# Kernel optimization log

Hardware: AMD Instinct MI355X
Metric: run time of the kernel (lower is better)

The kernel has to match this reference:

```python
import jax, jax.numpy as jnp
import numpy as np

B, S, D, H, F = 2, 2048, 1024, 16, 4096
DH = D // H  # per-head dim = 64
EPS = 1e-5


def _layer_norm(x, g, b):
    mu = jnp.mean(x, axis=-1, keepdims=True)
    var = jnp.mean((x - mu) ** 2, axis=-1, keepdims=True)
    return (x - mu) * jax.lax.rsqrt(var + EPS) * g + b


def _mha(q_in, kv_in, wq, bq, wk, bk, wv, bv, wo, bo, causal):
    b, s, d = q_in.shape
    q = (q_in @ wq + bq).reshape(b, s, H, DH).transpose(0, 2, 1, 3)
    k = (kv_in @ wk + bk).reshape(b, s, H, DH).transpose(0, 2, 1, 3)
    v = (kv_in @ wv + bv).reshape(b, s, H, DH).transpose(0, 2, 1, 3)
    scores = jnp.einsum('bhqd,bhkd->bhqk', q, k) / np.sqrt(DH).astype(np.float32)
    if causal:
        mask = jnp.tril(jnp.ones((s, s), dtype=bool))
        scores = jnp.where(mask, scores, -jnp.inf)
    attn = jax.nn.softmax(scores, axis=-1)
    out = jnp.einsum('bhqk,bhkd->bhqd', attn, v)
    out = out.transpose(0, 2, 1, 3).reshape(b, s, d)
    return out @ wo + bo


def setup_inputs() -> dict:
    key = jax.random.key(0)
    ks = iter(jax.random.split(key, 24))
    def w(shape, fan_in):
        return jax.random.normal(next(ks), shape, jnp.float32) / np.sqrt(fan_in).astype(np.float32)
    inp = {
        'encoder_output': jax.random.normal(next(ks), (B, S, D), jnp.float32),
        'decoder_input': jax.random.normal(next(ks), (B, S, D), jnp.float32),
    }
    for pre in ('sa', 'ca'):
        for nm in ('wq', 'wk', 'wv', 'wo'):
            inp[f'{pre}_{nm}'] = w((D, D), D)
            inp[f'{pre}_b{nm[-1]}'] = jnp.zeros((D,), jnp.float32)
        inp[f'{pre}_g'] = jnp.ones((D,), jnp.float32)
        inp[f'{pre}_bt'] = jnp.zeros((D,), jnp.float32)
    inp['f_w1'] = w((D, F), D); inp['f_b1'] = jnp.zeros((F,), jnp.float32)
    inp['f_w2'] = w((F, D), F); inp['f_b2'] = jnp.zeros((D,), jnp.float32)
    inp['f_g'] = jnp.ones((D,), jnp.float32); inp['f_bt'] = jnp.zeros((D,), jnp.float32)
    return inp


def reference(encoder_output, decoder_input,
              sa_wq, sa_bq, sa_wk, sa_bk, sa_wv, sa_bv, sa_wo, sa_bo, sa_g, sa_bt,
              ca_wq, ca_bq, ca_wk, ca_bk, ca_wv, ca_bv, ca_wo, ca_bo, ca_g, ca_bt,
              f_w1, f_b1, f_w2, f_b2, f_g, f_bt):
    # masked self-attention + residual + LN
    x = _mha(decoder_input, decoder_input, sa_wq, sa_bq, sa_wk, sa_bk, sa_wv, sa_bv, sa_wo, sa_bo, True)
    x = _layer_norm(x + decoder_input, sa_g, sa_bt)
    # encoder-decoder attention + residual + LN
    y = _mha(x, encoder_output, ca_wq, ca_bq, ca_wk, ca_bk, ca_wv, ca_bv, ca_wo, ca_bo, False)
    y = _layer_norm(y + x, ca_g, ca_bt)
    # FFN + residual + LN
    h = jax.nn.relu(y @ f_w1 + f_b1) @ f_w2 + f_b2
    return _layer_norm(h + y, f_g, f_bt)
```

## Files before the change

kernel.cpp:

```cpp
#include <hip/hip_runtime.h>
#include <hip/hip_bf16.h>


typedef __attribute__((ext_vector_type(8))) short bf16x8;
typedef __attribute__((ext_vector_type(4))) float f32x4;
typedef __attribute__((ext_vector_type(16))) float f32x16;

#define LOG2E 1.44269504088896340736f

constexpr int Bb = 2, Ss = 2048, Dd = 1024, Hh = 16, DHd = 64, Ff = 4096;
constexpr int Mrows = Bb * Ss;
constexpr int BHS = Bb * Hh * Ss;

static __device__ __forceinline__ ushort f2b(float f) {
    union { float f; unsigned u; } x{f};
    unsigned r = x.u + 0x7fffu + ((x.u >> 16) & 1u);
    return (ushort)(r >> 16);
}

static __device__ __forceinline__ unsigned pk2(float a, float b) {
    __hip_bfloat162 h = __float22bfloat162_rn(make_float2(a, b));
    unsigned u;
    __builtin_memcpy(&u, &h, 4);
    return u;
}

static __device__ __forceinline__ unsigned pk2t(float a, float b) {
    union { float f; unsigned u; } ua{a}, ub{b};
    return __builtin_amdgcn_perm(ub.u, ua.u, 0x07060302);
}

static __device__ __forceinline__ void gl2lds16(const void* g, void* l) {
    __builtin_amdgcn_global_load_lds(
        (const __attribute__((address_space(1))) void*)g,
        (__attribute__((address_space(3))) void*)l, 16, 0, 0);
}

__global__ __launch_bounds__(256) void cvt_kernel(const float* __restrict__ in,
                                                  ushort* __restrict__ out) {
    int i = (blockIdx.x * 256 + threadIdx.x) * 4;
    float4 v = *(const float4*)(in + i);
    ushort4 u;
    u.x = f2b(v.x); u.y = f2b(v.y); u.z = f2b(v.z); u.w = f2b(v.w);
    *(ushort4*)(out + i) = u;
}

__global__ __launch_bounds__(256) void wtrans_kernel(const float* __restrict__ w,
                                                     ushort* __restrict__ wT,
                                                     int K, int N) {
    __shared__ float t[32][33];
    int tx = threadIdx.x & 31, ty = threadIdx.x >> 5;
    int kb = blockIdx.y * 32, nb = blockIdx.x * 32;
#pragma unroll
    for (int i = 0; i < 4; i++)
        t[ty + i * 8][tx] = w[(size_t)(kb + ty + i * 8) * N + nb + tx];
    __syncthreads();
#pragma unroll
    for (int i = 0; i < 4; i++)
        wT[(size_t)(nb + ty + i * 8) * K + kb + tx] = f2b(t[tx][ty + i * 8]);
}

__global__ __launch_bounds__(256) void pack_bias(const float* __restrict__ a,
                                                 const float* __restrict__ b,
                                                 const float* __restrict__ c,
                                                 float* __restrict__ out) {
    int i = blockIdx.x * 256 + threadIdx.x;
    const float* src = a; int j = i;
    if (i >= 2048)      { src = c; j = i - 2048; }
    else if (i >= 1024) { src = b; j = i - 1024; }
    out[i] = src[j];
}

__global__ __launch_bounds__(256) void gemm_kernel(const ushort* __restrict__ A,
                                                   const ushort* __restrict__ BT,
                                                   const float* __restrict__ bias,
                                                   void* __restrict__ out,
                                                   int M, int N, int K, int klen,
                                                   int mode, int relu, float qsc,
                                                   int vwhich) {
    __shared__ __align__(16) ushort As[128 * 64];
    __shared__ __align__(16) ushort Bs[128 * 64];
    const int tid = threadIdx.x;
    const int lane = tid & 63, wave = tid >> 6;
    const int lr = lane & 15, quad = lane >> 4;
    const int wm = wave & 1, wn = wave >> 1;
    const int nwg = gridDim.x * gridDim.y;
    const int orig = blockIdx.y * gridDim.x + blockIdx.x;
    const int wg = (orig & 7) * (nwg >> 3) + (orig >> 3);
    const int m0 = (wg / gridDim.x) * 128, n0 = (wg % gridDim.x) * 128;
    const int kz = blockIdx.z;
    const int kstart = kz * klen;

    f32x4 acc[4][4];
#pragma unroll
    for (int i = 0; i < 4; i++)
#pragma unroll
        for (int j = 0; j < 4; j++) acc[i][j] = (f32x4){0.f, 0.f, 0.f, 0.f};

    const int srow = tid >> 3;
    const int gchunk = ((tid & 7) ^ (srow & 7)) * 8;
    const ushort* aBase = A + (size_t)(m0 + srow) * K + gchunk;
    const ushort* bBase = BT + (size_t)(n0 + srow) * K + gchunk;
    const size_t rowStep = (size_t)32 * K;

    const int slotA = ((quad) ^ (lr & 7)) * 8;
    const int slotB = ((4 + quad) ^ (lr & 7)) * 8;

    for (int k0 = kstart; k0 < kstart + klen; k0 += 64) {
#pragma unroll
        for (int c = 0; c < 4; c++) {
            gl2lds16(aBase + c * rowStep + k0, &As[c * 2048 + tid * 8]);
            gl2lds16(bBase + c * rowStep + k0, &Bs[c * 2048 + tid * 8]);
        }
        __syncthreads();
#pragma unroll
        for (int kk = 0; kk < 2; kk++) {
            const int slot = kk ? slotB : slotA;
            bf16x8 af[4], bfr[4];
#pragma unroll
            for (int i = 0; i < 4; i++)
                af[i] = *(const bf16x8*)&As[(wm * 64 + i * 16 + lr) * 64 + slot];
#pragma unroll
            for (int j = 0; j < 4; j++)
                bfr[j] = *(const bf16x8*)&Bs[(wn * 64 + j * 16 + lr) * 64 + slot];
#pragma unroll
            for (int i = 0; i < 4; i++)
#pragma unroll
                for (int j = 0; j < 4; j++)
                    acc[i][j] = __builtin_amdgcn_mfma_f32_16x16x32_bf16(af[i], bfr[j], acc[i][j], 0, 0, 0);
        }
        __syncthreads();
    }

#pragma unroll
    for (int j = 0; j < 4; j++) {
        int col = n0 + wn * 64 + j * 16 + lr;
        float bv = (bias && kz == 0) ? bias[col] : 0.f;
#pragma unroll
        for (int i = 0; i < 4; i++) {
            int row0 = m0 + wm * 64 + i * 16 + quad * 4;
            float v[4];
#pragma unroll
            for (int r = 0; r < 4; r++) {
                v[r] = acc[i][j][r] + bv;
                if (relu) v[r] = fmaxf(v[r], 0.f);
            }
            if (mode == 0) {
                float* op = (float*)out + (size_t)kz * M * N;
#pragma unroll
                for (int r = 0; r < 4; r++)
                    op[(size_t)(row0 + r) * N + col] = v[r];
            } else if (mode == 1) {
#pragma unroll
                for (int r = 0; r < 4; r++)
                    ((ushort*)out)[(size_t)(row0 + r) * N + col] = f2b(v[r]);
            } else {
                int which = col >> 10, n1 = col & 1023;
                int h = n1 >> 6, dh = n1 & 63;
                int b = row0 >> 11, s0 = row0 & 2047;
                size_t wbase = (size_t)which * (Bb * Hh * Ss * DHd);
                if (which == vwhich) {
                    uint2 pk;
                    pk.x = pk2(v[0], v[1]); pk.y = pk2(v[2], v[3]);
                    *(uint2*)((ushort*)out + wbase +
                              ((size_t)(b * Hh + h) * DHd + dh) * Ss + s0) = pk;
                } else {
                    float sc = (which == 0) ? qsc : 1.f;
#pragma unroll
                    for (int r = 0; r < 4; r++)
                        ((ushort*)out)[wbase + (((size_t)(b * Hh + h) * Ss + s0 + r) * DHd) + dh] =
                            f2b(v[r] * sc);
                }
            }
        }
    }
}

#define MFMAP(I0)                                                              \
    __builtin_amdgcn_s_setprio(1);                                             \
    _Pragma("unroll")                                                          \
    for (int j = 0; j < 4; j++) {                                              \
        acc[I0][j] = __builtin_amdgcn_mfma_f32_16x16x32_bf16(af[0][0], bfr[j][0], acc[I0][j], 0, 0, 0);         \
        acc[I0][j] = __builtin_amdgcn_mfma_f32_16x16x32_bf16(af[0][1], bfr[j][1], acc[I0][j], 0, 0, 0);         \
        acc[I0 + 1][j] = __builtin_amdgcn_mfma_f32_16x16x32_bf16(af[1][0], bfr[j][0], acc[I0 + 1][j], 0, 0, 0); \
        acc[I0 + 1][j] = __builtin_amdgcn_mfma_f32_16x16x32_bf16(af[1][1], bfr[j][1], acc[I0 + 1][j], 0, 0, 0); \
    }                                                                          \
    __builtin_amdgcn_s_setprio(0);

#define PHASE_READ_A(IB)                                                       \
    af[0][0] = *(const bf16x8*)&Ac[aoff0 + (IB) * 1024];                       \
    af[0][1] = *(const bf16x8*)&Ac[aoff1 + (IB) * 1024];                       \
    af[1][0] = *(const bf16x8*)&Ac[aoff0 + ((IB) + 1) * 1024];                 \
    af[1][1] = *(const bf16x8*)&Ac[aoff1 + ((IB) + 1) * 1024];

#define GTILE(PF)                                                              \
  {                                                                            \
    const ushort* Ac = &As[(t & 1) * 16384];                                   \
    const ushort* Bc = &Bs[(t & 1) * 16384];                                   \
    const int nb = (t & 1) ^ 1;                                                \
    const int kn = kstart + (t + 1) * 64;                                      \
    bf16x8 bfr[4][2], af[2][2];                                                \
                                                        \
    _Pragma("unroll")                                                          \
    for (int j = 0; j < 4; j++) {                                              \
        bfr[j][0] = *(const bf16x8*)&Bc[boff0 + j * 1024];                     \
        bfr[j][1] = *(const bf16x8*)&Bc[boff1 + j * 1024];                     \
    }                                                                          \
    PHASE_READ_A(0)                                                            \
    if (PF) { stB(nb, kn, 0); stB(nb, kn, 1); }                                \
    __builtin_amdgcn_s_barrier();                                              \
    asm volatile("s_waitcnt lgkmcnt(0)" ::: "memory");                         \
    MFMAP(0)                                                                   \
    __builtin_amdgcn_s_barrier();                                              \
                                                        \
    PHASE_READ_A(2)                                                            \
    if (PF) { stB(nb, kn, 2); stB(nb, kn, 3); }                                \
    __builtin_amdgcn_s_barrier();                                              \
    asm volatile("s_waitcnt lgkmcnt(0)" ::: "memory");                         \
    MFMAP(2)                                                                   \
    if (PF) asm volatile("s_waitcnt vmcnt(4)" ::: "memory");                   \
    else    asm volatile("s_waitcnt vmcnt(0)" ::: "memory");                   \
    __builtin_amdgcn_s_barrier();                                              \
                                                        \
    PHASE_READ_A(4)                                                            \
    if (PF) { stA(nb, kn, 0); stA(nb, kn, 2); }                                \
    __builtin_amdgcn_s_barrier();                                              \
    asm volatile("s_waitcnt lgkmcnt(0)" ::: "memory");                         \
    MFMAP(4)                                                                   \
    __builtin_amdgcn_s_barrier();                                              \
                                                        \
    PHASE_READ_A(6)                                                            \
    if (PF) { stA(nb, kn, 1); stA(nb, kn, 3); }                                \
    __builtin_amdgcn_s_barrier();                                              \
    asm volatile("s_waitcnt lgkmcnt(0)" ::: "memory");                         \
    MFMAP(6)                                                                   \
    if (PF) asm volatile("s_waitcnt vmcnt(2)" ::: "memory");                   \
    __builtin_amdgcn_s_barrier();                                              \
  }

__global__ __launch_bounds__(512) void gemm256(const ushort* __restrict__ A,
                                               const ushort* __restrict__ BT,
                                               const float* __restrict__ bias,
                                               void* __restrict__ out,
                                               int M, int N, int K, int klen,
                                               int mode, int relu, float qsc,
                                               int vwhich) {
    __shared__ __align__(16) ushort As[2 * 16384];
    __shared__ __align__(16) ushort Bs[2 * 16384];
    const int tid = threadIdx.x;
    const int lane = tid & 63, wave = tid >> 6;
    const int lr = lane & 15, quad = lane >> 4;
    const int wm = wave & 1, wn = wave >> 1;
    const int nwg = gridDim.x * gridDim.y;
    const int orig = blockIdx.y * gridDim.x + blockIdx.x;
    const int wg = (orig & 7) * (nwg >> 3) + (orig >> 3);
    const int m0 = (wg / gridDim.x) * 256, n0 = (wg % gridDim.x) * 256;
    const int kz = blockIdx.z;
    const int kstart = kz * klen;

    f32x4 acc[8][4];
#pragma unroll
    for (int i = 0; i < 8; i++)
#pragma unroll
        for (int j = 0; j < 4; j++) acc[i][j] = (f32x4){0.f, 0.f, 0.f, 0.f};

    const int srow = tid >> 3;
    const int gchunk = ((tid & 7) ^ (srow & 7)) * 8;
    const ushort* aBase = A + (size_t)(m0 + srow) * K + gchunk;
    const ushort* bBase = BT + (size_t)(n0 + srow) * K + gchunk;
    const size_t rowStep = (size_t)64 * K;

    auto stA = [&](int b, int kn, int c) {
        gl2lds16(aBase + (size_t)c * rowStep + kn, &As[b * 16384 + c * 4096 + tid * 8]);
    };
    auto stB = [&](int b, int kn, int c) {
        gl2lds16(bBase + (size_t)c * rowStep + kn, &Bs[b * 16384 + c * 4096 + tid * 8]);
    };

    const int aoff0 = (wm * 128 + lr) * 64 + (((0 * 4 + quad)) ^ (lr & 7)) * 8;
    const int aoff1 = (wm * 128 + lr) * 64 + (((1 * 4 + quad)) ^ (lr & 7)) * 8;
    const int boff0 = (wn * 64 + lr) * 64 + (((0 * 4 + quad)) ^ (lr & 7)) * 8;
    const int boff1 = (wn * 64 + lr) * 64 + (((1 * 4 + quad)) ^ (lr & 7)) * 8;

    stB(0, kstart, 0); stB(0, kstart, 1); stB(0, kstart, 2); stB(0, kstart, 3);
    stA(0, kstart, 0); stA(0, kstart, 2); stA(0, kstart, 1); stA(0, kstart, 3);
    asm volatile("s_waitcnt vmcnt(2)" ::: "memory");
    __builtin_amdgcn_s_barrier();

    const int nkt = klen >> 6;
    for (int t = 0; t < nkt - 1; t++) GTILE(1)
    { const int t = nkt - 1; GTILE(0) }

#pragma unroll
    for (int j = 0; j < 4; j++) {
        int col = n0 + wn * 64 + j * 16 + lr;
        float bv = (bias && kz == 0) ? bias[col] : 0.f;
#pragma unroll
        for (int i = 0; i < 8; i++) {
            int row0 = m0 + wm * 128 + i * 16 + quad * 4;
            float v[4];
#pragma unroll
            for (int r = 0; r < 4; r++) {
                v[r] = acc[i][j][r] + bv;
                if (relu) v[r] = fmaxf(v[r], 0.f);
            }
            if (mode == 0) {
                float* op = (float*)out + (size_t)kz * M * N;
#pragma unroll
                for (int r = 0; r < 4; r++)
                    op[(size_t)(row0 + r) * N + col] = v[r];
            } else if (mode == 1) {
#pragma unroll
                for (int r = 0; r < 4; r++)
                    ((ushort*)out)[(size_t)(row0 + r) * N + col] = f2b(v[r]);
            } else {
                int which = col >> 10, n1 = col & 1023;
                int h = n1 >> 6, dh = n1 & 63;
                int b = row0 >> 11, s0 = row0 & 2047;
                size_t wbase = (size_t)which * (Bb * Hh * Ss * DHd);
                if (which == vwhich) {
                    uint2 pk;
                    pk.x = pk2(v[0], v[1]); pk.y = pk2(v[2], v[3]);
                    *(uint2*)((ushort*)out + wbase +
                              ((size_t)(b * Hh + h) * DHd + dh) * Ss + s0) = pk;
                } else {
                    float sc = (which == 0) ? qsc : 1.f;
#pragma unroll
                    for (int r = 0; r < 4; r++)
                        ((ushort*)out)[wbase + (((size_t)(b * Hh + h) * Ss + s0 + r) * DHd) + dh] =
                            f2b(v[r] * sc);
                }
            }
        }
    }
}

__global__ __launch_bounds__(256, 2) void attn_kernel(const ushort* __restrict__ Q,
                                                      const ushort* __restrict__ Kg,
                                                      const ushort* __restrict__ VT,
                                                      float* __restrict__ Op0,
                                                      float* __restrict__ Op1,
                                                      float* __restrict__ Ml,
                                                      int causal) {
    __shared__ __align__(16) ushort Ks[64 * 64];
    __shared__ __align__(16) ushort Vs[64 * 64];
    const int tid = threadIdx.x;
    const int lane = tid & 63, w = tid >> 6;
    const int lr31 = lane & 31, hi = lane >> 5, l7 = lane & 7;
    const int hi4 = hi * 4;
    const int L = blockIdx.z * 256 + blockIdx.y * 8 + blockIdx.x;
    const int bh = (L & 7) | (((L >> 6) & 3) << 3);
    const int bx = (L >> 3) & 7;
    const int p = L >> 8;
    const int qt = causal ? (p ? bx : (7 - bx)) : bx;
    const size_t hb = (size_t)bh * Ss * DHd;
    const int qbase = qt * 256 + w * 64;

    bf16x8 qf[2][4];
#pragma unroll
    for (int qg = 0; qg < 2; qg++)
#pragma unroll
        for (int ks = 0; ks < 4; ks++)
            qf[qg][ks] = *(const bf16x8*)(Q + hb +
                (size_t)(qbase + qg * 32 + lr31) * DHd + ks * 16 + hi * 8);

    f32x16 o[2][2];
#pragma unroll
    for (int i = 0; i < 2; i++)
#pragma unroll
        for (int j = 0; j < 2; j++)
#pragma unroll
            for (int r = 0; r < 16; r++) o[i][j][r] = 0.f;
    float l0 = 0.f, l1 = 0.f;

    const int srow8 = tid >> 3, sslot = tid & 7;
    const int sswz = (sslot ^ (srow8 & 7)) * 8;
    const ushort* kSrc = Kg + hb + (size_t)srow8 * DHd + sswz;
    const ushort* vSrc = VT + hb + (size_t)srow8 * Ss + sswz;

    uint4 kr0, kr1, vr0, vr1;
    auto ldKV = [&](int k0) {
        kr0 = *(const uint4*)(kSrc + (size_t)(k0 +  0) * DHd);
        kr1 = *(const uint4*)(kSrc + (size_t)(k0 + 32) * DHd);
        vr0 = *(const uint4*)(vSrc + k0);
        vr1 = *(const uint4*)(vSrc + (size_t)32 * Ss + k0);
    };
    auto wrKV = [&]() {
        *(uint4*)&Ks[tid * 8]        = kr0;
        *(uint4*)&Ks[2048 + tid * 8] = kr1;
        *(uint4*)&Vs[tid * 8]        = vr0;
        *(uint4*)&Vs[2048 + tid * 8] = vr1;
    };

    int so[4];
#pragma unroll
    for (int ks = 0; ks < 4; ks++) so[ks] = ((ks * 2 + hi) ^ l7) * 8;

    const int ktEnd = causal ? (qt + 1) * 4 : (Ss / 64);

    ldKV(p * 64);
    wrKV();
    __syncthreads();

    for (int kt = p; kt < ktEnd; kt += 2) {
        const int k0 = kt * 64;
        const int pf = (kt + 2 < ktEnd);
        if (pf) ldKV((kt + 2) * 64);
        if (!causal || k0 <= qbase + 63) {
            bf16x8 pb[2][4];
            float ps0 = 0.f, ps1 = 0.f;
            const int maskT = causal && (k0 == qbase);
#pragma unroll
            for (int kg = 0; kg < 2; kg++) {
                bf16x8 kf[4];
#pragma unroll
                for (int ks = 0; ks < 4; ks++)
                    kf[ks] = *(const bf16x8*)&Ks[(kg * 32 + lr31) * 64 + so[ks]];
                f32x16 st[2];
#pragma unroll
                for (int qg = 0; qg < 2; qg++) {
#pragma unroll
                    for (int r = 0; r < 16; r++) st[qg][r] = 0.f;
#pragma unroll
                    for (int ks = 0; ks < 4; ks++)
                        st[qg] = __builtin_amdgcn_mfma_f32_32x32x16_bf16(
                            kf[ks], qf[qg][ks], st[qg], 0, 0, 0);
                }
                if (maskT) {
#pragma unroll
                    for (int r = 0; r < 16; r++) {
                        int klr = kg * 32 + (r & 3) + 8 * (r >> 2) + hi4;
                        st[0][r] = (klr > lr31) ? -1e30f : st[0][r];
                        st[1][r] = (klr > lr31 + 32) ? -1e30f : st[1][r];
                    }
                }
#pragma unroll
                for (int qg = 0; qg < 2; qg++) {
                    float pv[16];
#pragma unroll
                    for (int r = 0; r < 16; r++) {
                        pv[r] = __builtin_amdgcn_exp2f(fminf(st[qg][r], 88.f));
                        if (qg == 0) ps0 += pv[r]; else ps1 += pv[r];
                    }
#pragma unroll
                    for (int tt = 0; tt < 2; tt++) {
                        const int rb = tt * 8;
                        unsigned X0 = pk2t(pv[rb + 0], pv[rb + 1]);
                        unsigned X1 = pk2t(pv[rb + 2], pv[rb + 3]);
                        unsigned Y0 = pk2t(pv[rb + 4], pv[rb + 5]);
                        unsigned Y1 = pk2t(pv[rb + 6], pv[rb + 7]);
                        asm("v_permlane32_swap_b32 %0, %1" : "+v"(X0), "+v"(Y0));
                        asm("v_permlane32_swap_b32 %0, %1" : "+v"(X1), "+v"(Y1));
                        union { unsigned u[4]; bf16x8 v; } pw;
                        pw.u[0] = X0; pw.u[1] = X1; pw.u[2] = Y0; pw.u[3] = Y1;
                        pb[qg][kg * 2 + tt] = pw.v;
                    }
                }
            }
            l0 += ps0 + __shfl_xor(ps0, 32);
            l1 += ps1 + __shfl_xor(ps1, 32);
#pragma unroll
            for (int ks = 0; ks < 4; ks++) {
                bf16x8 av0 = *(const bf16x8*)&Vs[lr31 * 64 + so[ks]];
                bf16x8 av1 = *(const bf16x8*)&Vs[(32 + lr31) * 64 + so[ks]];
                o[0][0] = __builtin_amdgcn_mfma_f32_32x32x16_bf16(av0, pb[0][ks], o[0][0], 0, 0, 0);
                o[0][1] = __builtin_amdgcn_mfma_f32_32x32x16_bf16(av1, pb[0][ks], o[0][1], 0, 0, 0);
                o[1][0] = __builtin_amdgcn_mfma_f32_32x32x16_bf16(av0, pb[1][ks], o[1][0], 0, 0, 0);
                o[1][1] = __builtin_amdgcn_mfma_f32_32x32x16_bf16(av1, pb[1][ks], o[1][1], 0, 0, 0);
            }
        }
        if (pf) {
            __syncthreads();
            wrKV();
            __syncthreads();
        }
    }

    Ml[(size_t)p * BHS + (size_t)bh * Ss + qbase + lane] = (lane & 32) ? l1 : l0;
    float* Op = p ? Op1 : Op0;
#pragma unroll
    for (int qg = 0; qg < 2; qg++) {
        size_t ob = ((size_t)bh * Ss + qbase + qg * 32 + lr31) * 64;
#pragma unroll
        for (int dhg = 0; dhg < 2; dhg++)
#pragma unroll
            for (int rq = 0; rq < 4; rq++) {
                f32x4 t;
#pragma unroll
                for (int c = 0; c < 4; c++) t[c] = o[qg][dhg][rq * 4 + c];
                *(f32x4*)(Op + ob + dhg * 32 + rq * 8 + hi4) = t;
            }
    }
}

__global__ __launch_bounds__(256) void attn_combine(const float* __restrict__ Op0,
                                                    const float* __restrict__ Op1,
                                                    const float* __restrict__ Ml,
                                                    ushort* __restrict__ O) {
    int g = blockIdx.x * 256 + threadIdx.x;
    int q = g >> 4, seg = g & 15;
    float inv = 1.f / (Ml[q] + Ml[BHS + q]);
    f32x4 x = *(const f32x4*)(Op0 + (size_t)q * 64 + seg * 4);
    f32x4 y = *(const f32x4*)(Op1 + (size_t)q * 64 + seg * 4);
    int bh = q >> 11, sq = q & 2047, bb = bh >> 4, h = bh & 15;
    uint2 u;
    u.x = pk2((x[0] + y[0]) * inv, (x[1] + y[1]) * inv);
    u.y = pk2((x[2] + y[2]) * inv, (x[3] + y[3]) * inv);
    *(uint2*)(O + ((size_t)(bb * Ss + sq)) * Dd + h * 64 + seg * 4) = u;
}

__global__ __launch_bounds__(256) void ln_kernel(const float* __restrict__ a0,
                                                 const float* __restrict__ a1,
                                                 const float* __restrict__ a2,
                                                 const float* __restrict__ a3,
                                                 const float* __restrict__ resid,
                                                 const float* __restrict__ g,
                                                 const float* __restrict__ bt,
                                                 float* __restrict__ out32,
                                                 ushort* __restrict__ outb) {
    const int row = blockIdx.x, tid = threadIdx.x;
    const size_t base = (size_t)row * Dd + tid * 4;
    float4 av = *(const float4*)(a0 + base);
    if (a1) { float4 t = *(const float4*)(a1 + base); av.x += t.x; av.y += t.y; av.z += t.z; av.w += t.w; }
    if (a2) { float4 t = *(const float4*)(a2 + base); av.x += t.x; av.y += t.y; av.z += t.z; av.w += t.w; }
    if (a3) { float4 t = *(const float4*)(a3 + base); av.x += t.x; av.y += t.y; av.z += t.z; av.w += t.w; }
    float4 rv = *(const float4*)(resid + base);
    float x0 = av.x + rv.x, x1 = av.y + rv.y, x2 = av.z + rv.z, x3 = av.w + rv.w;
    float s = x0 + x1 + x2 + x3;
    float q = x0 * x0 + x1 * x1 + x2 * x2 + x3 * x3;
#pragma unroll
    for (int off = 1; off <= 32; off <<= 1) {
        s += __shfl_xor(s, off);
        q += __shfl_xor(q, off);
    }
    __shared__ float red[8];
    int wave = tid >> 6, lane = tid & 63;
    if (lane == 0) { red[wave] = s; red[4 + wave] = q; }
    __syncthreads();
    s = red[0] + red[1] + red[2] + red[3];
    q = red[4] + red[5] + red[6] + red[7];
    float mu = s * (1.f / Dd);
    float var = q * (1.f / Dd) - mu * mu;
    float rs = rsqrtf(var + 1e-5f);
    int col = tid * 4;
    float4 gv = *(const float4*)(g + col);
    float4 bv = *(const float4*)(bt + col);
    float y0 = (x0 - mu) * rs * gv.x + bv.x;
    float y1 = (x1 - mu) * rs * gv.y + bv.y;
    float y2 = (x2 - mu) * rs * gv.z + bv.z;
    float y3 = (x3 - mu) * rs * gv.w + bv.w;
    if (out32) *(float4*)(out32 + base) = make_float4(y0, y1, y2, y3);
    if (outb) {
        ushort4 u; u.x = f2b(y0); u.y = f2b(y1); u.z = f2b(y2); u.w = f2b(y3);
        *(ushort4*)(outb + base) = u;
    }
}

constexpr size_t OFF_XB     = 0;
constexpr size_t OFF_ENCB   = OFF_XB     + 8388608;
constexpr size_t OFF_QKVWT  = OFF_ENCB   + 8388608;
constexpr size_t OFF_CAWQT  = OFF_QKVWT  + 6291456;
constexpr size_t OFF_CAKVT  = OFF_CAWQT  + 2097152;
constexpr size_t OFF_SAWOT  = OFF_CAKVT  + 4194304;
constexpr size_t OFF_CAWOT  = OFF_SAWOT  + 2097152;
constexpr size_t OFF_FW1T   = OFF_CAWOT  + 2097152;
constexpr size_t OFF_FW2T   = OFF_FW1T   + 8388608;
constexpr size_t OFF_SABQKV = OFF_FW2T   + 8388608;
constexpr size_t OFF_CABKV  = OFF_SABQKV + 12288;
constexpr size_t OFF_QB     = OFF_CABKV  + 8192;
constexpr size_t OFF_KB     = OFF_QB     + 8388608;
constexpr size_t OFF_VB     = OFF_KB     + 8388608;
constexpr size_t OFF_ATTNO  = OFF_VB     + 8388608;
constexpr size_t OFF_F1     = OFF_ATTNO  + 8388608;
constexpr size_t OFF_F2     = OFF_F1     + 16777216;
constexpr size_t OFF_X1B    = OFF_F2     + 16777216;
constexpr size_t OFF_F3     = OFF_X1B    + 8388608;
constexpr size_t OFF_YB     = OFF_F3     + 16777216;
constexpr size_t OFF_H1B    = OFF_YB     + 8388608;

extern "C" void kernel_launch(void* const* d_in, const int* in_sizes, int n_in,
                              void* d_out, int out_size, void* d_ws, size_t ws_size,
                              hipStream_t stream) {
    const float* enc   = (const float*)d_in[0];
    const float* dec   = (const float*)d_in[1];
    const float* sa_wq = (const float*)d_in[2];
    const float* sa_bq = (const float*)d_in[3];
    const float* sa_wk = (const float*)d_in[4];
    const float* sa_bk = (const float*)d_in[5];
    const float* sa_wv = (const float*)d_in[6];
    const float* sa_bv = (const float*)d_in[7];
    const float* sa_wo = (const float*)d_in[8];
    const float* sa_bo = (const float*)d_in[9];
    const float* sa_g  = (const float*)d_in[10];
    const float* sa_bt = (const float*)d_in[11];
    const float* ca_wq = (const float*)d_in[12];
    const float* ca_bq = (const float*)d_in[13];
    const float* ca_wk = (const float*)d_in[14];
    const float* ca_bk = (const float*)d_in[15];
    const float* ca_wv = (const float*)d_in[16];
    const float* ca_bv = (const float*)d_in[17];
    const float* ca_wo = (const float*)d_in[18];
    const float* ca_bo = (const float*)d_in[19];
    const float* ca_g  = (const float*)d_in[20];
    const float* ca_bt = (const float*)d_in[21];
    const float* f_w1  = (const float*)d_in[22];
    const float* f_b1  = (const float*)d_in[23];
    const float* f_w2  = (const float*)d_in[24];
    const float* f_b2  = (const float*)d_in[25];
    const float* f_g   = (const float*)d_in[26];
    const float* f_bt  = (const float*)d_in[27];

    char* ws = (char*)d_ws;
    ushort* xb     = (ushort*)(ws + OFF_XB);
    ushort* encb   = (ushort*)(ws + OFF_ENCB);
    ushort* qkvwT  = (ushort*)(ws + OFF_QKVWT);
    ushort* cawqT  = (ushort*)(ws + OFF_CAWQT);
    ushort* cakvT  = (ushort*)(ws + OFF_CAKVT);
    ushort* sawoT  = (ushort*)(ws + OFF_SAWOT);
    ushort* cawoT  = (ushort*)(ws + OFF_CAWOT);
    ushort* fw1T   = (ushort*)(ws + OFF_FW1T);
    ushort* fw2T   = (ushort*)(ws + OFF_FW2T);
    float*  sabqkv = (float*)(ws + OFF_SABQKV);
    float*  cabkv  = (float*)(ws + OFF_CABKV);
    ushort* qb     = (ushort*)(ws + OFF_QB);
    ushort* kb     = (ushort*)(ws + OFF_KB);
    ushort* vbt    = (ushort*)(ws + OFF_VB);
    ushort* attno  = (ushort*)(ws + OFF_ATTNO);
    float*  f1     = (float*)(ws + OFF_F1);
    float*  f2     = (float*)(ws + OFF_F2);
    ushort* x1b    = (ushort*)(ws + OFF_X1B);
    float*  x1f    = (float*)(ws + OFF_F3);
    ushort* yb     = (ushort*)(ws + OFF_YB);
    ushort* h1b    = (ushort*)(ws + OFF_H1B);
    float*  yfp    = (float*)(ws + OFF_QB);
    float*  ml     = (float*)(ws + OFF_H1B);

    const float QSC = 0.125f * LOG2E;
    const size_t MN = (size_t)Mrows * Dd;

    cvt_kernel<<<4096, 256, 0, stream>>>(dec, xb);
    cvt_kernel<<<4096, 256, 0, stream>>>(enc, encb);
    dim3 tgDD(32, 32);
    wtrans_kernel<<<tgDD, 256, 0, stream>>>(sa_wq, qkvwT,                 Dd, Dd);
    wtrans_kernel<<<tgDD, 256, 0, stream>>>(sa_wk, qkvwT + 1024 * 1024,   Dd, Dd);
    wtrans_kernel<<<tgDD, 256, 0, stream>>>(sa_wv, qkvwT + 2 * 1024 * 1024, Dd, Dd);
    wtrans_kernel<<<tgDD, 256, 0, stream>>>(sa_wo, sawoT,                 Dd, Dd);
    wtrans_kernel<<<tgDD, 256, 0, stream>>>(ca_wq, cawqT,                 Dd, Dd);
    wtrans_kernel<<<tgDD, 256, 0, stream>>>(ca_wk, cakvT,                 Dd, Dd);
    wtrans_kernel<<<tgDD, 256, 0, stream>>>(ca_wv, cakvT + 1024 * 1024,   Dd, Dd);
    wtrans_kernel<<<tgDD, 256, 0, stream>>>(ca_wo, cawoT,                 Dd, Dd);
    wtrans_kernel<<<dim3(128, 32), 256, 0, stream>>>(f_w1, fw1T, Dd, Ff);
    wtrans_kernel<<<dim3(32, 128), 256, 0, stream>>>(f_w2, fw2T, Ff, Dd);
    pack_bias<<<12, 256, 0, stream>>>(sa_bq, sa_bk, sa_bv, sabqkv);
    pack_bias<<<8, 256, 0, stream>>>(ca_bk, ca_bv, nullptr, cabkv);

    gemm256<<<dim3(12, 16, 1), 512, 0, stream>>>(xb, qkvwT, sabqkv, qb,
                                                 Mrows, 3072, Dd, Dd, 2, 0, QSC, 2);
    attn_kernel<<<dim3(8, 32, 2), 256, 0, stream>>>(qb, kb, vbt, f1, x1f, ml, 1);
    attn_combine<<<4096, 256, 0, stream>>>(f1, x1f, ml, attno);
    gemm_kernel<<<dim3(8, 32, 2), 256, 0, stream>>>(attno, sawoT, sa_bo, f1,
                                                    Mrows, Dd, Dd, 512, 0, 0, 1.f, -1);
    ln_kernel<<<4096, 256, 0, stream>>>(f1, f2, nullptr, nullptr, dec,
                                        sa_g, sa_bt, x1f, x1b);

    gemm_kernel<<<dim3(8, 32, 1), 256, 0, stream>>>(x1b, cawqT, ca_bq, qb,
                                                    Mrows, Dd, Dd, Dd, 2, 0, QSC, -1);
    gemm256<<<dim3(8, 16, 1), 512, 0, stream>>>(encb, cakvT, cabkv, kb,
                                                Mrows, 2048, Dd, Dd, 2, 0, 1.f, 1);
    attn_kernel<<<dim3(8, 32, 2), 256, 0, stream>>>(qb, kb, vbt, f1, f2, ml, 0);
    attn_combine<<<4096, 256, 0, stream>>>(f1, f2, ml, attno);
    gemm_kernel<<<dim3(8, 32, 2), 256, 0, stream>>>(attno, cawoT, ca_bo, f1,
                                                    Mrows, Dd, Dd, 512, 0, 0, 1.f, -1);
    ln_kernel<<<4096, 256, 0, stream>>>(f1, f2, nullptr, nullptr, x1f,
                                        ca_g, ca_bt, yfp, yb);

    gemm256<<<dim3(16, 16, 1), 512, 0, stream>>>(yb, fw1T, f_b1, h1b,
                                                 Mrows, Ff, Dd, Dd, 1, 1, 1.f, -1);
    gemm256<<<dim3(4, 16, 4), 512, 0, stream>>>(h1b, fw2T, f_b2, f1,
                                                Mrows, Dd, Ff, 1024, 0, 0, 1.f, -1);
    ln_kernel<<<4096, 256, 0, stream>>>(f1, f1 + MN, f1 + 2 * MN, f1 + 3 * MN, yfp,
                                        f_g, f_bt, (float*)d_out, nullptr);
}
```

Before: 559.9 us.

## Split attention key range four ways and raise MFMA wave priority

The attention kernel now splits each query tile's key loop across four partitions instead of two, launching twice as many blocks, each striding by four key tiles. The combine kernel sums four partial outputs and four row sums, and workspace buffers are reassigned to hold the extra partials. It also wraps the MFMA sections in s_setprio and drops the clamp before exp2. The aim is more parallelism and better MFMA issue, at the cost of more partial-output traffic, a heavier combine, and possible aliasing hazards with the reused workspace.

```diff
diff --git a/kernel.cpp b/kernel.cpp
--- a/kernel.cpp
+++ b/kernel.cpp
@@ -340,6 +340,8 @@
                                                       const ushort* __restrict__ VT,
                                                       float* __restrict__ Op0,
                                                       float* __restrict__ Op1,
+                                                      float* __restrict__ Op2,
+                                                      float* __restrict__ Op3,
                                                       float* __restrict__ Ml,
                                                       int causal) {
     __shared__ __align__(16) ushort Ks[64 * 64];
@@ -352,7 +354,7 @@
     const int bh = (L & 7) | (((L >> 6) & 3) << 3);
     const int bx = (L >> 3) & 7;
     const int p = L >> 8;
-    const int qt = causal ? (p ? bx : (7 - bx)) : bx;
+    const int qt = causal ? ((p & 1) ? bx : (7 - bx)) : bx;
     const size_t hb = (size_t)bh * Ss * DHd;
     const int qbase = qt * 256 + w * 64;
 
@@ -402,10 +404,10 @@
     wrKV();
     __syncthreads();
 
-    for (int kt = p; kt < ktEnd; kt += 2) {
+    for (int kt = p; kt < ktEnd; kt += 4) {
         const int k0 = kt * 64;
-        const int pf = (kt + 2 < ktEnd);
-        if (pf) ldKV((kt + 2) * 64);
+        const int pf = (kt + 4 < ktEnd);
+        if (pf) ldKV((kt + 4) * 64);
         if (!causal || k0 <= qbase + 63) {
             bf16x8 pb[2][4];
             float ps0 = 0.f, ps1 = 0.f;
@@ -421,11 +423,16 @@
                 for (int qg = 0; qg < 2; qg++) {
 #pragma unroll
                     for (int r = 0; r < 16; r++) st[qg][r] = 0.f;
+                }
+                __builtin_amdgcn_s_setprio(1);
+#pragma unroll
+                for (int qg = 0; qg < 2; qg++) {
 #pragma unroll
                     for (int ks = 0; ks < 4; ks++)
                         st[qg] = __builtin_amdgcn_mfma_f32_32x32x16_bf16(
                             kf[ks], qf[qg][ks], st[qg], 0, 0, 0);
                 }
+                __builtin_amdgcn_s_setprio(0);
                 if (maskT) {
 #pragma unroll
                     for (int r = 0; r < 16; r++) {
@@ -439,7 +446,7 @@
                     float pv[16];
 #pragma unroll
                     for (int r = 0; r < 16; r++) {
-                        pv[r] = __builtin_amdgcn_exp2f(fminf(st[qg][r], 88.f));
+                        pv[r] = __builtin_amdgcn_exp2f(st[qg][r]);
                         if (qg == 0) ps0 += pv[r]; else ps1 += pv[r];
                     }
 #pragma unroll
@@ -459,6 +466,7 @@
             }
             l0 += ps0 + __shfl_xor(ps0, 32);
             l1 += ps1 + __shfl_xor(ps1, 32);
+            __builtin_amdgcn_s_setprio(1);
 #pragma unroll
             for (int ks = 0; ks < 4; ks++) {
                 bf16x8 av0 = *(const bf16x8*)&Vs[lr31 * 64 + so[ks]];
@@ -468,6 +476,7 @@
                 o[1][0] = __builtin_amdgcn_mfma_f32_32x32x16_bf16(av0, pb[1][ks], o[1][0], 0, 0, 0);
                 o[1][1] = __builtin_amdgcn_mfma_f32_32x32x16_bf16(av1, pb[1][ks], o[1][1], 0, 0, 0);
             }
+            __builtin_amdgcn_s_setprio(0);
         }
         if (pf) {
             __syncthreads();
@@ -477,7 +486,7 @@
     }
 
     Ml[(size_t)p * BHS + (size_t)bh * Ss + qbase + lane] = (lane & 32) ? l1 : l0;
-    float* Op = p ? Op1 : Op0;
+    float* Op = (p == 0) ? Op0 : (p == 1) ? Op1 : (p == 2) ? Op2 : Op3;
 #pragma unroll
     for (int qg = 0; qg < 2; qg++) {
         size_t ob = ((size_t)bh * Ss + qbase + qg * 32 + lr31) * 64;
@@ -495,17 +504,22 @@
 
 __global__ __launch_bounds__(256) void attn_combine(const float* __restrict__ Op0,
                                                     const float* __restrict__ Op1,
+                                                    const float* __restrict__ Op2,
+                                                    const float* __restrict__ Op3,
                                                     const float* __restrict__ Ml,
                                                     ushort* __restrict__ O) {
     int g = blockIdx.x * 256 + threadIdx.x;
     int q = g >> 4, seg = g & 15;
-    float inv = 1.f / (Ml[q] + Ml[BHS + q]);
-    f32x4 x = *(const f32x4*)(Op0 + (size_t)q * 64 + seg * 4);
-    f32x4 y = *(const f32x4*)(Op1 + (size_t)q * 64 + seg * 4);
+    float inv = 1.f / (Ml[q] + Ml[BHS + q] + Ml[2 * BHS + q] + Ml[3 * BHS + q]);
+    size_t off = (size_t)q * 64 + seg * 4;
+    f32x4 x = *(const f32x4*)(Op0 + off);
+    f32x4 y = *(const f32x4*)(Op1 + off);
+    f32x4 z = *(const f32x4*)(Op2 + off);
+    f32x4 u4 = *(const f32x4*)(Op3 + off);
     int bh = q >> 11, sq = q & 2047, bb = bh >> 4, h = bh & 15;
     uint2 u;
-    u.x = pk2((x[0] + y[0]) * inv, (x[1] + y[1]) * inv);
-    u.y = pk2((x[2] + y[2]) * inv, (x[3] + y[3]) * inv);
+    u.x = pk2((x[0] + y[0] + z[0] + u4[0]) * inv, (x[1] + y[1] + z[1] + u4[1]) * inv);
+    u.y = pk2((x[2] + y[2] + z[2] + u4[2]) * inv, (x[3] + y[3] + z[3] + u4[3]) * inv);
     *(uint2*)(O + ((size_t)(bb * Ss + sq)) * Dd + h * 64 + seg * 4) = u;
 }
 
@@ -633,7 +647,9 @@
     ushort* yb     = (ushort*)(ws + OFF_YB);
     ushort* h1b    = (ushort*)(ws + OFF_H1B);
     float*  yfp    = (float*)(ws + OFF_QB);
-    float*  ml     = (float*)(ws + OFF_H1B);
+    float*  op2    = (float*)(ws + OFF_YB);
+    float*  op3    = (float*)(ws + OFF_H1B + 8388608);
+    float*  ml     = (float*)(ws + OFF_X1B);
 
     const float QSC = 0.125f * LOG2E;
     const size_t MN = (size_t)Mrows * Dd;
@@ -656,8 +672,8 @@
 
     gemm256<<<dim3(12, 16, 1), 512, 0, stream>>>(xb, qkvwT, sabqkv, qb,
                                                  Mrows, 3072, Dd, Dd, 2, 0, QSC, 2);
-    attn_kernel<<<dim3(8, 32, 2), 256, 0, stream>>>(qb, kb, vbt, f1, x1f, ml, 1);
-    attn_combine<<<4096, 256, 0, stream>>>(f1, x1f, ml, attno);
+    attn_kernel<<<dim3(8, 32, 4), 256, 0, stream>>>(qb, kb, vbt, f1, f2, op2, op3, ml, 1);
+    attn_combine<<<4096, 256, 0, stream>>>(f1, f2, op2, op3, ml, attno);
     gemm_kernel<<<dim3(8, 32, 2), 256, 0, stream>>>(attno, sawoT, sa_bo, f1,
                                                     Mrows, Dd, Dd, 512, 0, 0, 1.f, -1);
     ln_kernel<<<4096, 256, 0, stream>>>(f1, f2, nullptr, nullptr, dec,
@@ -667,8 +683,8 @@
                                                     Mrows, Dd, Dd, Dd, 2, 0, QSC, -1);
     gemm256<<<dim3(8, 16, 1), 512, 0, stream>>>(encb, cakvT, cabkv, kb,
                                                 Mrows, 2048, Dd, Dd, 2, 0, 1.f, 1);
-    attn_kernel<<<dim3(8, 32, 2), 256, 0, stream>>>(qb, kb, vbt, f1, f2, ml, 0);
-    attn_combine<<<4096, 256, 0, stream>>>(f1, f2, ml, attno);
+    attn_kernel<<<dim3(8, 32, 4), 256, 0, stream>>>(qb, kb, vbt, f1, f2, op2, op3, ml, 0);
+    attn_combine<<<4096, 256, 0, stream>>>(f1, f2, op2, op3, ml, attno);
     gemm_kernel<<<dim3(8, 32, 2), 256, 0, stream>>>(attno, cawoT, ca_bo, f1,
                                                     Mrows, Dd, Dd, 512, 0, 0, 1.f, -1);
     ln_kernel<<<4096, 256, 0, stream>>>(f1, f2, nullptr, nullptr, x1f,
```

Measured after the change: 588.0 us. 1.05x slower.
